# Kernel optimization log

Measured on AMD Instinct MI355X. Metric: run time of the kernel, lower is better.

The kernel has to match this reference:

```python
import jax, jax.numpy as jnp
import numpy as np

B, F, D = 4096, 32, 32
LAYER_SIZE = [128, 128]


def setup_inputs() -> dict:
    key = jax.random.key(0)
    k1, k2, k3 = jax.random.split(key, 3)
    inputs = jax.random.normal(k1, (B, F, D), dtype=jnp.float32)
    # CIN filters: shape [1, field_nums[0]*field_nums[i], field_nums[i+1]]
    field_nums = [F] + LAYER_SIZE
    filter_0 = (jax.random.normal(k2, (1, field_nums[0] * field_nums[0], field_nums[1]), dtype=jnp.float32) * 0.05)
    filter_1 = (jax.random.normal(k3, (1, field_nums[0] * field_nums[1], field_nums[2]), dtype=jnp.float32) * 0.05)
    return {"inputs": inputs, "filter_0": filter_0, "filter_1": filter_1}


def _cin_forward(inputs, filters):
    x0 = inputs          # [B, F, D] -- hidden_nn_layers[0]
    prev = inputs        # hidden_nn_layers[-1]
    outs = []
    for W in filters:    # W: [1, F*M, N]
        # outer product over field dims: [B, F, M, D]
        z = jnp.einsum('bhd,bmd->bhmd', x0, prev)
        b, h, m, d = z.shape
        z = z.reshape(b, h * m, d)                 # [B, F*M, D]
        # 1x1 conv over the F*M axis == contraction with W[0]: [F*M, N]
        cur = jnp.einsum('bpd,pn->bnd', z, W[0])   # [B, N, D]
        cur = jax.nn.relu(cur)
        prev = cur
        outs.append(cur)
    result = jnp.concatenate(outs, axis=1)         # [B, sum(layer_size), D]
    return jnp.sum(result, axis=-1)                # [B, sum(layer_size)]


def reference(inputs, filter_0, filter_1):
    return _cin_forward(inputs, (filter_0, filter_1))
```

## Files before the change

### kernel.cpp

```cpp
#include <hip/hip_runtime.h>


typedef _Float16 half_t;
typedef _Float16 half4v __attribute__((ext_vector_type(4)));
typedef _Float16 half8 __attribute__((ext_vector_type(8)));
typedef float f32x16 __attribute__((ext_vector_type(16)));

__global__ void prep_w_kernel(const float* __restrict__ W0,
                              const float* __restrict__ W1,
                              half_t* __restrict__ Wp0,
                              half_t* __restrict__ Wp1) {
  int gid = blockIdx.x * 256 + threadIdx.x;
  int n = gid & 127;
  int tg = (gid >> 7) & 1;
  int s = gid >> 8;
  const float* W;
  half_t* Wp;
  int M, sl;
  if (s < 64) { W = W0; Wp = Wp0; M = 32; sl = s; }
  else        { W = W1; Wp = Wp1; M = 128; sl = s - 64; }
  int h = sl & 31, mc = sl >> 5;
  int kbase = h * M + mc * 16 + tg * 8;
  half8 v;
#pragma unroll
  for (int j = 0; j < 8; ++j) v[j] = (half_t)W[(size_t)(kbase + j) * 128 + n];
  *(half8*)(Wp + ((size_t)(sl * 2 + tg) * 128 + n) * 8) = v;
}

__device__ __forceinline__ int pswz(int row, int m) {
  return row * 128 + (((m >> 3) ^ (row & 15)) << 3) + (m & 7);
}

__device__ __forceinline__ f32x16 mfma3216(half8 a, half8 b, f32x16 c) {
  return __builtin_amdgcn_mfma_f32_32x32x16_f16(a, b, c, 0, 0, 0);
}

template <int MC, bool L1>
__device__ __forceinline__ void layer_loop(const half_t* __restrict__ Wp,
                                           const half_t* __restrict__ psrc,
                                           const half_t* __restrict__ xQw,
                                           int woff0, int woff1, int rowb,
                                           int l31, int hi, f32x16 acc[4][2]) {
  half8 B0a0 = *(const half8*)(Wp + 0 * 2048 + woff0);
  half8 B0a1 = *(const half8*)(Wp + 0 * 2048 + woff1);
  half8 B1a0 = *(const half8*)(Wp + 1 * 2048 + woff0);
  half8 B1a1 = *(const half8*)(Wp + 1 * 2048 + woff1);
  half8 B0b0 = *(const half8*)(Wp + 2 * 2048 + woff0);
  half8 B0b1 = *(const half8*)(Wp + 2 * 2048 + woff1);
  half8 B1b0 = *(const half8*)(Wp + 3 * 2048 + woff0);
  half8 B1b1 = *(const half8*)(Wp + 3 * 2048 + woff1);
  half8 xqa = *(const half8*)(xQw);
  half8 xqb = *(const half8*)(xQw + 256);

  half8 P[4];
#pragma unroll
  for (int rt = 0; rt < 4; ++rt)
    P[rt] = L1 ? *(const half8*)&psrc[(rowb + rt * 32 + l31) * 40 + hi * 8]
               : *(const half8*)&psrc[pswz(rowb + rt * 32 + l31, hi * 8)];

#pragma unroll 1
  for (int mc = 0; mc < MC; ++mc) {
#pragma unroll 1
    for (int p = 0; p < 8; ++p) {
      const int g0 = mc * 16 + 2 * p;
#pragma unroll
      for (int rt = 0; rt < 4; ++rt) {
        half8 Af = P[rt] * xqa[rt * 2 + 0];
        acc[rt][0] = mfma3216(Af, B0a0, acc[rt][0]);
        acc[rt][1] = mfma3216(Af, B0a1, acc[rt][1]);
      }
#pragma unroll
      for (int rt = 0; rt < 4; ++rt) {
        half8 Af = P[rt] * xqa[rt * 2 + 1];
        acc[rt][0] = mfma3216(Af, B1a0, acc[rt][0]);
        acc[rt][1] = mfma3216(Af, B1a1, acc[rt][1]);
      }
      {
        const int sn = (2 * (g0 + 2)) & (MC * 32 - 1);
        B0a0 = *(const half8*)(Wp + (size_t)sn * 2048 + woff0);
        B0a1 = *(const half8*)(Wp + (size_t)sn * 2048 + woff1);
        B1a0 = *(const half8*)(Wp + (size_t)(sn + 1) * 2048 + woff0);
        B1a1 = *(const half8*)(Wp + (size_t)(sn + 1) * 2048 + woff1);
        xqa = *(const half8*)(xQw + ((2 * p + 2) & 15) * 256);
      }
#pragma unroll
      for (int rt = 0; rt < 4; ++rt) {
        half8 Af = P[rt] * xqb[rt * 2 + 0];
        acc[rt][0] = mfma3216(Af, B0b0, acc[rt][0]);
        acc[rt][1] = mfma3216(Af, B0b1, acc[rt][1]);
      }
#pragma unroll
      for (int rt = 0; rt < 4; ++rt) {
        half8 Af = P[rt] * xqb[rt * 2 + 1];
        acc[rt][0] = mfma3216(Af, B1b0, acc[rt][0]);
        acc[rt][1] = mfma3216(Af, B1b1, acc[rt][1]);
      }
      {
        const int sn = (2 * (g0 + 3)) & (MC * 32 - 1);
        B0b0 = *(const half8*)(Wp + (size_t)sn * 2048 + woff0);
        B0b1 = *(const half8*)(Wp + (size_t)sn * 2048 + woff1);
        B1b0 = *(const half8*)(Wp + (size_t)(sn + 1) * 2048 + woff0);
        B1b1 = *(const half8*)(Wp + (size_t)(sn + 1) * 2048 + woff1);
        xqb = *(const half8*)(xQw + ((2 * p + 3) & 15) * 256);
      }
    }
    if (mc + 1 < MC) {
      const int mn = (mc + 1) * 16;
#pragma unroll
      for (int rt = 0; rt < 4; ++rt)
        P[rt] = L1 ? *(const half8*)&psrc[(rowb + rt * 32 + l31) * 40 + mn +
                                          hi * 8]
                   : *(const half8*)&psrc[pswz(rowb + rt * 32 + l31,
                                               mn + hi * 8)];
    }
  }
}

__global__ __launch_bounds__(256, 2) void cin_fused_kernel(
    const float* __restrict__ x0,
    const half_t* __restrict__ Wp0,
    const half_t* __restrict__ Wp1,
    float* __restrict__ out) {
  __shared__ half_t xQ[2 * 16 * 32 * 8];
  __shared__ half_t prevT[8 * 32 * 128];
  half_t* xT = prevT;

  const int tid = threadIdx.x;
  const int b0 = blockIdx.x * 8;

  const float4* x4 = (const float4*)(x0 + (size_t)b0 * 1024);
#pragma unroll
  for (int r = 0; r < 8; ++r) {
    int q = r * 256 + tid;
    float4 v = x4[q];
    int e4 = q * 4;
    int bi = e4 >> 10, h = (e4 >> 5) & 31, d0 = e4 & 31;
    half4v hv = {(half_t)v.x, (half_t)v.y, (half_t)v.z, (half_t)v.w};
    const int quad = bi >> 2, rtl = bi & 3;
#pragma unroll
    for (int j = 0; j < 4; ++j) {
      xQ[quad * 4096 + (h >> 1) * 256 + (d0 + j) * 8 + rtl * 2 + (h & 1)] =
          hv[j];
      xT[(bi * 32 + d0 + j) * 40 + h] = hv[j];
    }
  }
  __syncthreads();

  const int lane = tid & 63;
  const int l31 = lane & 31;
  const int hi = lane >> 5;
  const int wave = tid >> 6;
  const int wr = wave >> 1;
  const int wc = wave & 1;

  const int woff0 = hi * 1024 + (wc * 64 + l31) * 8;
  const int woff1 = hi * 1024 + (wc * 64 + 32 + l31) * 8;
  const int rowb = wr * 128;
  const half_t* xQw = xQ + wr * 4096 + l31 * 8;

  f32x16 acc[4][2];
#pragma unroll
  for (int rt = 0; rt < 4; ++rt)
#pragma unroll
    for (int ct = 0; ct < 2; ++ct)
#pragma unroll
      for (int r = 0; r < 16; ++r) acc[rt][ct][r] = 0.f;

  layer_loop<2, true>(Wp0, xT, xQw, woff0, woff1, rowb, l31, hi, acc);

  __syncthreads();

#pragma unroll
  for (int rt = 0; rt < 4; ++rt) {
#pragma unroll
    for (int ct = 0; ct < 2; ++ct) {
      float s = 0.f;
#pragma unroll
      for (int r = 0; r < 16; ++r) {
        float v = acc[rt][ct][r];
        v = v > 0.f ? v : 0.f;
        s += v;
        int d = (r & 3) + ((r >> 2) << 3) + hi * 4;
        prevT[pswz(rowb + rt * 32 + d, wc * 64 + ct * 32 + l31)] = (half_t)v;
        acc[rt][ct][r] = 0.f;
      }
      s += __shfl_down(s, 32);
      if (lane < 32)
        out[(size_t)(b0 + wr * 4 + rt) * 256 + wc * 64 + ct * 32 + lane] = s;
    }
  }
  __syncthreads();

  layer_loop<8, false>(Wp1, prevT, xQw, woff0, woff1, rowb, l31, hi, acc);

#pragma unroll
  for (int rt = 0; rt < 4; ++rt) {
#pragma unroll
    for (int ct = 0; ct < 2; ++ct) {
      float s = 0.f;
#pragma unroll
      for (int r = 0; r < 16; ++r) {
        float v = acc[rt][ct][r];
        s += v > 0.f ? v : 0.f;
      }
      s += __shfl_down(s, 32);
      if (lane < 32)
        out[(size_t)(b0 + wr * 4 + rt) * 256 + 128 + wc * 64 + ct * 32 +
            lane] = s;
    }
  }
}

extern "C" void kernel_launch(void* const* d_in, const int* in_sizes, int n_in,
                              void* d_out, int out_size, void* d_ws,
                              size_t ws_size, hipStream_t stream) {
  const float* x0 = (const float*)d_in[0];
  const float* w0 = (const float*)d_in[1];
  const float* w1 = (const float*)d_in[2];
  float* out = (float*)d_out;
  char* ws = (char*)d_ws;

  half_t* Wp0 = (half_t*)(ws);
  half_t* Wp1 = (half_t*)(ws + 64 * 2048 * 2);

  hipLaunchKernelGGL(prep_w_kernel, dim3(320), dim3(256), 0, stream, w0, w1,
                     Wp0, Wp1);
  hipLaunchKernelGGL(cin_fused_kernel, dim3(512), dim3(256), 0, stream, x0,
                     Wp0, Wp1, out);
}
```

Measured before the change: 193.8 us.

## Halve per-block batch tile to 4 and drop software-pipelined weight prefetch

Each block now processes 4 batch rows instead of 8, so per-wave accumulator tiles shrink from 4x2 to 2x2 and shared memory is halved. Launch bounds rise to 4 blocks per SM and the grid doubles to 1024 blocks, aiming for higher occupancy to hide latency. The explicit register double-buffering of weight and xQ fragments is removed; loads are issued just before use, relying on occupancy instead. The cost is that each weight fragment loaded from global/L2 is reused across half as many MFMAs, doubling weight traffic per unit of work.

```diff
diff --git a/kernel.cpp b/kernel.cpp
--- a/kernel.cpp
+++ b/kernel.cpp
@@ -40,21 +40,10 @@
                                            const half_t* __restrict__ psrc,
                                            const half_t* __restrict__ xQw,
                                            int woff0, int woff1, int rowb,
-                                           int l31, int hi, f32x16 acc[4][2]) {
-  half8 B0a0 = *(const half8*)(Wp + 0 * 2048 + woff0);
-  half8 B0a1 = *(const half8*)(Wp + 0 * 2048 + woff1);
-  half8 B1a0 = *(const half8*)(Wp + 1 * 2048 + woff0);
-  half8 B1a1 = *(const half8*)(Wp + 1 * 2048 + woff1);
-  half8 B0b0 = *(const half8*)(Wp + 2 * 2048 + woff0);
-  half8 B0b1 = *(const half8*)(Wp + 2 * 2048 + woff1);
-  half8 B1b0 = *(const half8*)(Wp + 3 * 2048 + woff0);
-  half8 B1b1 = *(const half8*)(Wp + 3 * 2048 + woff1);
-  half8 xqa = *(const half8*)(xQw);
-  half8 xqb = *(const half8*)(xQw + 256);
-
-  half8 P[4];
-#pragma unroll
-  for (int rt = 0; rt < 4; ++rt)
+                                           int l31, int hi, f32x16 acc[2][2]) {
+  half8 P[2];
+#pragma unroll
+  for (int rt = 0; rt < 2; ++rt)
     P[rt] = L1 ? *(const half8*)&psrc[(rowb + rt * 32 + l31) * 40 + hi * 8]
                : *(const half8*)&psrc[pswz(rowb + rt * 32 + l31, hi * 8)];
 
@@ -62,52 +51,49 @@
   for (int mc = 0; mc < MC; ++mc) {
 #pragma unroll 1
     for (int p = 0; p < 8; ++p) {
-      const int g0 = mc * 16 + 2 * p;
-#pragma unroll
-      for (int rt = 0; rt < 4; ++rt) {
-        half8 Af = P[rt] * xqa[rt * 2 + 0];
-        acc[rt][0] = mfma3216(Af, B0a0, acc[rt][0]);
-        acc[rt][1] = mfma3216(Af, B0a1, acc[rt][1]);
-      }
-#pragma unroll
-      for (int rt = 0; rt < 4; ++rt) {
-        half8 Af = P[rt] * xqa[rt * 2 + 1];
-        acc[rt][0] = mfma3216(Af, B1a0, acc[rt][0]);
-        acc[rt][1] = mfma3216(Af, B1a1, acc[rt][1]);
-      }
+      const int sb = mc * 32 + 4 * p;
+      half8 xq = *(const half8*)(xQw + p * 256);
       {
-        const int sn = (2 * (g0 + 2)) & (MC * 32 - 1);
-        B0a0 = *(const half8*)(Wp + (size_t)sn * 2048 + woff0);
-        B0a1 = *(const half8*)(Wp + (size_t)sn * 2048 + woff1);
-        B1a0 = *(const half8*)(Wp + (size_t)(sn + 1) * 2048 + woff0);
-        B1a1 = *(const half8*)(Wp + (size_t)(sn + 1) * 2048 + woff1);
-        xqa = *(const half8*)(xQw + ((2 * p + 2) & 15) * 256);
-      }
-#pragma unroll
-      for (int rt = 0; rt < 4; ++rt) {
-        half8 Af = P[rt] * xqb[rt * 2 + 0];
-        acc[rt][0] = mfma3216(Af, B0b0, acc[rt][0]);
-        acc[rt][1] = mfma3216(Af, B0b1, acc[rt][1]);
-      }
-#pragma unroll
-      for (int rt = 0; rt < 4; ++rt) {
-        half8 Af = P[rt] * xqb[rt * 2 + 1];
-        acc[rt][0] = mfma3216(Af, B1b0, acc[rt][0]);
-        acc[rt][1] = mfma3216(Af, B1b1, acc[rt][1]);
+        half8 B00 = *(const half8*)(Wp + (size_t)(sb + 0) * 2048 + woff0);
+        half8 B01 = *(const half8*)(Wp + (size_t)(sb + 0) * 2048 + woff1);
+        half8 B10 = *(const half8*)(Wp + (size_t)(sb + 1) * 2048 + woff0);
+        half8 B11 = *(const half8*)(Wp + (size_t)(sb + 1) * 2048 + woff1);
+        half8 A00 = P[0] * xq[0];
+        half8 A10 = P[1] * xq[2];
+        half8 A01 = P[0] * xq[1];
+        half8 A11 = P[1] * xq[3];
+        acc[0][0] = mfma3216(A00, B00, acc[0][0]);
+        acc[0][1] = mfma3216(A00, B01, acc[0][1]);
+        acc[1][0] = mfma3216(A10, B00, acc[1][0]);
+        acc[1][1] = mfma3216(A10, B01, acc[1][1]);
+        acc[0][0] = mfma3216(A01, B10, acc[0][0]);
+        acc[0][1] = mfma3216(A01, B11, acc[0][1]);
+        acc[1][0] = mfma3216(A11, B10, acc[1][0]);
+        acc[1][1] = mfma3216(A11, B11, acc[1][1]);
       }
       {
-        const int sn = (2 * (g0 + 3)) & (MC * 32 - 1);
-        B0b0 = *(const half8*)(Wp + (size_t)sn * 2048 + woff0);
-        B0b1 = *(const half8*)(Wp + (size_t)sn * 2048 + woff1);
-        B1b0 = *(const half8*)(Wp + (size_t)(sn + 1) * 2048 + woff0);
-        B1b1 = *(const half8*)(Wp + (size_t)(sn + 1) * 2048 + woff1);
-        xqb = *(const half8*)(xQw + ((2 * p + 3) & 15) * 256);
+        half8 B00 = *(const half8*)(Wp + (size_t)(sb + 2) * 2048 + woff0);
+        half8 B01 = *(const half8*)(Wp + (size_t)(sb + 2) * 2048 + woff1);
+        half8 B10 = *(const half8*)(Wp + (size_t)(sb + 3) * 2048 + woff0);
+        half8 B11 = *(const half8*)(Wp + (size_t)(sb + 3) * 2048 + woff1);
+        half8 A00 = P[0] * xq[4];
+        half8 A10 = P[1] * xq[6];
+        half8 A01 = P[0] * xq[5];
+        half8 A11 = P[1] * xq[7];
+        acc[0][0] = mfma3216(A00, B00, acc[0][0]);
+        acc[0][1] = mfma3216(A00, B01, acc[0][1]);
+        acc[1][0] = mfma3216(A10, B00, acc[1][0]);
+        acc[1][1] = mfma3216(A10, B01, acc[1][1]);
+        acc[0][0] = mfma3216(A01, B10, acc[0][0]);
+        acc[0][1] = mfma3216(A01, B11, acc[0][1]);
+        acc[1][0] = mfma3216(A11, B10, acc[1][0]);
+        acc[1][1] = mfma3216(A11, B11, acc[1][1]);
       }
     }
     if (mc + 1 < MC) {
       const int mn = (mc + 1) * 16;
 #pragma unroll
-      for (int rt = 0; rt < 4; ++rt)
+      for (int rt = 0; rt < 2; ++rt)
         P[rt] = L1 ? *(const half8*)&psrc[(rowb + rt * 32 + l31) * 40 + mn +
                                           hi * 8]
                    : *(const half8*)&psrc[pswz(rowb + rt * 32 + l31,
@@ -116,30 +102,31 @@
   }
 }
 
-__global__ __launch_bounds__(256, 2) void cin_fused_kernel(
+__global__ __launch_bounds__(256, 4) void cin_fused_kernel(
     const float* __restrict__ x0,
     const half_t* __restrict__ Wp0,
     const half_t* __restrict__ Wp1,
     float* __restrict__ out) {
-  __shared__ half_t xQ[2 * 16 * 32 * 8];
-  __shared__ half_t prevT[8 * 32 * 128];
+  __shared__ half_t xQ[2 * 8 * 32 * 8];
+  __shared__ half_t prevT[4 * 32 * 128];
   half_t* xT = prevT;
 
   const int tid = threadIdx.x;
-  const int b0 = blockIdx.x * 8;
+  const int b0 = blockIdx.x * 4;
 
   const float4* x4 = (const float4*)(x0 + (size_t)b0 * 1024);
 #pragma unroll
-  for (int r = 0; r < 8; ++r) {
+  for (int r = 0; r < 4; ++r) {
     int q = r * 256 + tid;
     float4 v = x4[q];
     int e4 = q * 4;
     int bi = e4 >> 10, h = (e4 >> 5) & 31, d0 = e4 & 31;
     half4v hv = {(half_t)v.x, (half_t)v.y, (half_t)v.z, (half_t)v.w};
-    const int quad = bi >> 2, rtl = bi & 3;
+    const int pair = bi >> 1, rtl = bi & 1;
+    const int pp = h >> 2, hpar = (h >> 1) & 1, par = h & 1;
 #pragma unroll
     for (int j = 0; j < 4; ++j) {
-      xQ[quad * 4096 + (h >> 1) * 256 + (d0 + j) * 8 + rtl * 2 + (h & 1)] =
+      xQ[pair * 2048 + pp * 256 + (d0 + j) * 8 + hpar * 4 + rtl * 2 + par] =
           hv[j];
       xT[(bi * 32 + d0 + j) * 40 + h] = hv[j];
     }
@@ -155,12 +142,12 @@
 
   const int woff0 = hi * 1024 + (wc * 64 + l31) * 8;
   const int woff1 = hi * 1024 + (wc * 64 + 32 + l31) * 8;
-  const int rowb = wr * 128;
-  const half_t* xQw = xQ + wr * 4096 + l31 * 8;
-
-  f32x16 acc[4][2];
-#pragma unroll
-  for (int rt = 0; rt < 4; ++rt)
+  const int rowb = wr * 64;
+  const half_t* xQw = xQ + wr * 2048 + l31 * 8;
+
+  f32x16 acc[2][2];
+#pragma unroll
+  for (int rt = 0; rt < 2; ++rt)
 #pragma unroll
     for (int ct = 0; ct < 2; ++ct)
 #pragma unroll
@@ -171,7 +158,7 @@
   __syncthreads();
 
 #pragma unroll
-  for (int rt = 0; rt < 4; ++rt) {
+  for (int rt = 0; rt < 2; ++rt) {
 #pragma unroll
     for (int ct = 0; ct < 2; ++ct) {
       float s = 0.f;
@@ -186,7 +173,7 @@
       }
       s += __shfl_down(s, 32);
       if (lane < 32)
-        out[(size_t)(b0 + wr * 4 + rt) * 256 + wc * 64 + ct * 32 + lane] = s;
+        out[(size_t)(b0 + wr * 2 + rt) * 256 + wc * 64 + ct * 32 + lane] = s;
     }
   }
   __syncthreads();
@@ -194,7 +181,7 @@
   layer_loop<8, false>(Wp1, prevT, xQw, woff0, woff1, rowb, l31, hi, acc);
 
 #pragma unroll
-  for (int rt = 0; rt < 4; ++rt) {
+  for (int rt = 0; rt < 2; ++rt) {
 #pragma unroll
     for (int ct = 0; ct < 2; ++ct) {
       float s = 0.f;
@@ -205,7 +192,7 @@
       }
       s += __shfl_down(s, 32);
       if (lane < 32)
-        out[(size_t)(b0 + wr * 4 + rt) * 256 + 128 + wc * 64 + ct * 32 +
+        out[(size_t)(b0 + wr * 2 + rt) * 256 + 128 + wc * 64 + ct * 32 +
             lane] = s;
     }
   }
@@ -225,6 +212,6 @@
 
   hipLaunchKernelGGL(prep_w_kernel, dim3(320), dim3(256), 0, stream, w0, w1,
                      Wp0, Wp1);
-  hipLaunchKernelGGL(cin_fused_kernel, dim3(512), dim3(256), 0, stream, x0,
+  hipLaunchKernelGGL(cin_fused_kernel, dim3(1024), dim3(256), 0, stream, x0,
                      Wp0, Wp1, out);
 }
```

Result: slower. 230.8 us (+19.1%).
